# Performance work log

Hardware: AMD Instinct MI355X
Metric: run time of the kernel (lower is better)

The kernel has to match this reference:

```python
import jax, jax.numpy as jnp
import numpy as np

EPS = 1e-5

@jax.custom_vjp
def binarize(x):
    # sign binarization used by Conv2d_1w1a (1-bit weights and activations)
    return jnp.where(x >= 0, 1.0, -1.0).astype(x.dtype)

def _bin_fwd(x):
    return binarize(x), x

def _bin_bwd(x, g):
    # straight-through estimator with hardtanh clipping (standard BNN STE)
    return (g * (jnp.abs(x) <= 1.0).astype(g.dtype),)

binarize.defvjp(_bin_fwd, _bin_bwd)

def setup_inputs() -> dict:
    key = jax.random.key(0)
    k1, k2, k3 = jax.random.split(key, 3)
    B, C_in, H, W = 32, 256, 56, 56
    C_half = 512 // 2
    x = jax.random.normal(k1, (B, C_in, H, W), dtype=jnp.float32)
    gamma = jnp.ones((C_in,), dtype=jnp.float32)
    beta = jnp.zeros((C_in,), dtype=jnp.float32)
    w1 = jax.random.normal(k2, (C_half, C_in), dtype=jnp.float32) * 0.05
    w2 = jax.random.normal(k3, (C_half, C_in), dtype=jnp.float32) * 0.05
    return {"x": x, "gamma": gamma, "beta": beta, "w1": w1, "w2": w2}

def reference(x, gamma, beta, w1, w2):
    # BatchNorm2d (training mode: batch statistics, biased variance)
    mean = jnp.mean(x, axis=(0, 2, 3), keepdims=True)
    var = jnp.var(x, axis=(0, 2, 3), keepdims=True)
    xn = (x - mean) * jax.lax.rsqrt(var + EPS)
    xn = xn * gamma[None, :, None, None] + beta[None, :, None, None]

    # binarize activations once; both convs consume the same binarized map
    a = binarize(xn)
    b1 = binarize(w1)  # [C_half, C_in]
    b2 = binarize(w2)

    # 1x1 stride-2 conv == strided slice + channel contraction
    a1 = a[:, :, ::2, ::2]      # conv_1 path
    a2 = a[:, :, 1::2, 1::2]    # conv_2 path on out[:, :, 1:, 1:]

    out1 = jnp.einsum('bchw,oc->bohw', a1, b1)
    out2 = jnp.einsum('bchw,oc->bohw', a2, b2)
    return jnp.concatenate([out1, out2], axis=1)
```

## Files before the change

kernel.cpp:

```cpp
#include <hip/hip_runtime.h>
#include <stdint.h>

#define CIN 256
#define HW  3136
#define HW4 784
#define NB  32
#define NHO 28
#define NWO 28

__global__ void k_stats_partial(const float* __restrict__ x, double* __restrict__ part) {
    int blk = blockIdx.x;
    int c = blk >> 3;
    int chunk = blk & 7;
    int tid = threadIdx.x;
    double s = 0.0, sq = 0.0;
    for (int bq = 0; bq < 4; ++bq) {
        int b = chunk * 4 + bq;
        const float4* base = (const float4*)x + (size_t)(b * CIN + c) * HW4;
        for (int i = tid; i < HW4; i += 256) {
            float4 v = base[i];
            double a0 = v.x, a1 = v.y, a2 = v.z, a3 = v.w;
            s  += (a0 + a1) + (a2 + a3);
            sq += (a0*a0 + a1*a1) + (a2*a2 + a3*a3);
        }
    }
    __shared__ double ls[256], lq[256];
    ls[tid] = s; lq[tid] = sq;
    __syncthreads();
    for (int off = 128; off > 0; off >>= 1) {
        if (tid < off) { ls[tid] += ls[tid+off]; lq[tid] += lq[tid+off]; }
        __syncthreads();
    }
    if (tid == 0) {
        part[blk*2]   = ls[0];
        part[blk*2+1] = lq[0];
    }
}

__global__ void k_finalize(const double* __restrict__ part,
                           const float* __restrict__ gamma, const float* __restrict__ beta,
                           const float* __restrict__ w1, const float* __restrict__ w2,
                           double* __restrict__ mean_d, double* __restrict__ sg_d,
                           double* __restrict__ beta_d,
                           unsigned long long* __restrict__ wp) {
    int blk = blockIdx.x;
    int tid = threadIdx.x;
    if (blk == 512) {
        int c = tid;
        double s = 0.0, sq = 0.0;
        for (int k = 0; k < 8; ++k) {
            s  += part[(c*8+k)*2];
            sq += part[(c*8+k)*2+1];
        }
        const double n = 100352.0;
        double mean = s / n;
        double var  = sq / n - mean*mean;
        if (var < 0.0) var = 0.0;
        double invstd = 1.0 / sqrt(var + 1e-5);
        mean_d[c] = mean;
        sg_d[c]   = invstd * (double)gamma[c];
        beta_d[c] = (double)beta[c];
    } else {
        int wave = tid >> 6, l = tid & 63;
        int w_idx = blk * 4 + wave;
        int p = w_idx >> 10;
        int rem = w_idx & 1023;
        int o = rem >> 2, wv = rem & 3;
        const float* w = p ? w2 : w1;
        float v = w[o*256 + wv*64 + l];
        unsigned long long m = __ballot(v >= 0.0f);
        if (l == 0) wp[w_idx] = m;
    }
}

__global__ void k_binpack(const float* __restrict__ x,
                          const double* __restrict__ mean_d, const double* __restrict__ sg_d,
                          const double* __restrict__ beta_d,
                          unsigned long long* __restrict__ ap) {
    __shared__ double smean[256], ssg[256], sbeta[256];
    __shared__ unsigned char pred[256*116];
    int blk = blockIdx.x;
    int b = blk / NHO, ho = blk % NHO;
    int tid = threadIdx.x;
    smean[tid] = mean_d[tid]; ssg[tid] = sg_d[tid]; sbeta[tid] = beta_d[tid];
    __syncthreads();

    uint32_t* pred32 = (uint32_t*)pred;
    #pragma unroll 4
    for (int k = 0; k < 28; ++k) {
        int i4 = tid + k*256;
        int c  = i4 / 28;
        int r4 = i4 - c*28;
        float4 v = ((const float4*)x)[(size_t)(b*CIN + c)*HW4 + ho*28 + r4];
        double m = smean[c], sg = ssg[c], bt = sbeta[c];
        uint32_t bits = 0;
        bits |= (((double)v.x - m)*sg + bt >= 0.0) ? 0x00000001u : 0u;
        bits |= (((double)v.y - m)*sg + bt >= 0.0) ? 0x00000100u : 0u;
        bits |= (((double)v.z - m)*sg + bt >= 0.0) ? 0x00010000u : 0u;
        bits |= (((double)v.w - m)*sg + bt >= 0.0) ? 0x01000000u : 0u;
        pred32[c*29 + r4] = bits;
    }
    __syncthreads();

    int g = tid >> 6, l = tid & 63;
    int c = g*64 + l;
    for (int p = 0; p < 2; ++p) {
        for (int wo = 0; wo < NWO; ++wo) {
            unsigned char pr = pred[c*116 + p*57 + 2*wo];
            unsigned long long mask = __ballot(pr != 0);
            if (l == 0)
                ap[(size_t)(((p*NB + b)*NHO + ho)*NWO + wo)*4 + g] = mask;
        }
    }
}

__global__ void k_bingemm(const unsigned long long* __restrict__ ap,
                          const unsigned long long* __restrict__ wp,
                          float* __restrict__ out) {
    __shared__ unsigned long long wl[2048];
    int tid = threadIdx.x;
    for (int k = tid; k < 2048; k += 256) wl[k] = wp[k];
    int blk = blockIdx.x;
    int b = blk / NHO, ho = blk % NHO;
    int o_sub = tid >> 5, wi = tid & 31;
    bool act = wi < NWO;
    unsigned long long a0[2][4];
    if (act) {
        for (int p = 0; p < 2; ++p)
            #pragma unroll
            for (int j = 0; j < 4; ++j)
                a0[p][j] = ap[(size_t)(((p*NB + b)*NHO + ho)*NWO + wi)*4 + j];
    }
    __syncthreads();
    if (!act) return;
    for (int p = 0; p < 2; ++p) {
        size_t outbase = ((size_t)(b*512 + p*256) * 784) + (size_t)ho*NWO + wi;
        #pragma unroll 4
        for (int og = 0; og < 32; ++og) {
            int o = og*8 + o_sub;
            const unsigned long long* w = &wl[p*1024 + o*4];
            int d = __popcll(a0[p][0]^w[0]) + __popcll(a0[p][1]^w[1])
                  + __popcll(a0[p][2]^w[2]) + __popcll(a0[p][3]^w[3]);
            out[outbase + (size_t)o*784] = (float)(256 - 2*d);
        }
    }
}

extern "C" void kernel_launch(void* const* d_in, const int* in_sizes, int n_in,
                              void* d_out, int out_size, void* d_ws, size_t ws_size,
                              hipStream_t stream) {
    const float* x     = (const float*)d_in[0];
    const float* gamma = (const float*)d_in[1];
    const float* beta  = (const float*)d_in[2];
    const float* w1    = (const float*)d_in[3];
    const float* w2    = (const float*)d_in[4];
    float* out = (float*)d_out;

    char* ws = (char*)d_ws;
    double* part   = (double*)ws;
    double* mean_d = (double*)(ws + 32768);
    double* sg_d   = (double*)(ws + 34816);
    double* beta_d = (double*)(ws + 36864);
    unsigned long long* wp = (unsigned long long*)(ws + 40960);
    unsigned long long* ap = (unsigned long long*)(ws + 57344);

    k_stats_partial<<<2048, 256, 0, stream>>>(x, part);
    k_finalize<<<513, 256, 0, stream>>>(part, gamma, beta, w1, w2, mean_d, sg_d, beta_d, wp);
    k_binpack<<<NB*NHO, 256, 0, stream>>>(x, mean_d, sg_d, beta_d, ap);
    k_bingemm<<<NB*NHO, 256, 0, stream>>>(ap, wp, out);
}
```

Baseline: 216.4 us.

## Fuse four kernels into two: stats+weight pack, then finalize+binpack+popcount GEMM

Weight bit-packing moves into the stats kernel as extra blocks. BN finalize, activation bit-packing and the XNOR-popcount GEMM merge into one kernel that keeps packed activations in shared memory instead of a global round trip. Only the strided pixels actually used are kept in the shared predicate buffer, which shrinks its footprint. Each fused block now recomputes the per-channel finalize redundantly and holds more shared memory, which may reduce occupancy.

Measured after the change: 206.0 us. 4.8% less time.

```diff
diff --git a/kernel.cpp b/kernel.cpp
--- a/kernel.cpp
+++ b/kernel.cpp
@@ -2,139 +2,129 @@
 #include <stdint.h>
 
 #define CIN 256
-#define HW  3136
 #define HW4 784
 #define NB  32
 #define NHO 28
 #define NWO 28
 
-__global__ void k_stats_partial(const float* __restrict__ x, double* __restrict__ part) {
+__global__ __launch_bounds__(256) void k_stage1(const float* __restrict__ x,
+                          const float* __restrict__ w1, const float* __restrict__ w2,
+                          double* __restrict__ part, unsigned long long* __restrict__ wp) {
     int blk = blockIdx.x;
-    int c = blk >> 3;
-    int chunk = blk & 7;
     int tid = threadIdx.x;
-    double s = 0.0, sq = 0.0;
-    for (int bq = 0; bq < 4; ++bq) {
-        int b = chunk * 4 + bq;
-        const float4* base = (const float4*)x + (size_t)(b * CIN + c) * HW4;
-        for (int i = tid; i < HW4; i += 256) {
-            float4 v = base[i];
-            double a0 = v.x, a1 = v.y, a2 = v.z, a3 = v.w;
-            s  += (a0 + a1) + (a2 + a3);
-            sq += (a0*a0 + a1*a1) + (a2*a2 + a3*a3);
+    if (blk < 2048) {
+        int c = blk >> 3, chunk = blk & 7;
+        double s = 0.0, sq = 0.0;
+        for (int bq = 0; bq < 4; ++bq) {
+            int b = chunk * 4 + bq;
+            const float4* base = (const float4*)x + (size_t)(b * CIN + c) * HW4;
+            for (int i = tid; i < HW4; i += 256) {
+                float4 v = base[i];
+                double a0 = v.x, a1 = v.y, a2 = v.z, a3 = v.w;
+                s  += (a0 + a1) + (a2 + a3);
+                sq += (a0*a0 + a1*a1) + (a2*a2 + a3*a3);
+            }
         }
-    }
-    __shared__ double ls[256], lq[256];
-    ls[tid] = s; lq[tid] = sq;
-    __syncthreads();
-    for (int off = 128; off > 0; off >>= 1) {
-        if (tid < off) { ls[tid] += ls[tid+off]; lq[tid] += lq[tid+off]; }
+        __shared__ double ls[256], lq[256];
+        ls[tid] = s; lq[tid] = sq;
         __syncthreads();
-    }
-    if (tid == 0) {
-        part[blk*2]   = ls[0];
-        part[blk*2+1] = lq[0];
+        for (int off = 128; off > 0; off >>= 1) {
+            if (tid < off) { ls[tid] += ls[tid+off]; lq[tid] += lq[tid+off]; }
+            __syncthreads();
+        }
+        if (tid == 0) {
+            part[(chunk*256 + c)*2]   = ls[0];
+            part[(chunk*256 + c)*2+1] = lq[0];
+        }
+    } else {
+        int wave = tid >> 6, l = tid & 63;
+        int baseTask = ((blk - 2048)*4 + wave)*4;
+        #pragma unroll
+        for (int t = 0; t < 4; ++t) {
+            int w_idx = baseTask + t;
+            int p = w_idx >> 10, rem = w_idx & 1023;
+            int o = rem >> 2, wv = rem & 3;
+            const float* w = p ? w2 : w1;
+            float v = w[o*256 + wv*64 + l];
+            unsigned long long m = __ballot(v >= 0.0f);
+            if (l == 0) wp[w_idx] = m;
+        }
     }
 }
 
-__global__ void k_finalize(const double* __restrict__ part,
-                           const float* __restrict__ gamma, const float* __restrict__ beta,
-                           const float* __restrict__ w1, const float* __restrict__ w2,
-                           double* __restrict__ mean_d, double* __restrict__ sg_d,
-                           double* __restrict__ beta_d,
-                           unsigned long long* __restrict__ wp) {
+__global__ __launch_bounds__(256) void k_fused(const float* __restrict__ x,
+    const double* __restrict__ part, const float* __restrict__ gamma,
+    const float* __restrict__ beta, const unsigned long long* __restrict__ wp,
+    float* __restrict__ out) {
+    __shared__ double sm[256], ssg[256], sbt[256];
+    __shared__ unsigned char pred[256*60];
+    __shared__ unsigned long long wl[2048];
+    __shared__ unsigned long long apl[224];
     int blk = blockIdx.x;
+    int b = blk / NHO, ho = blk % NHO;
     int tid = threadIdx.x;
-    if (blk == 512) {
+
+    {
+        const ulonglong2* src = (const ulonglong2*)wp;
+        ulonglong2* dst = (ulonglong2*)wl;
+        for (int k = tid; k < 1024; k += 256) dst[k] = src[k];
+    }
+    {
         int c = tid;
         double s = 0.0, sq = 0.0;
         for (int k = 0; k < 8; ++k) {
-            s  += part[(c*8+k)*2];
-            sq += part[(c*8+k)*2+1];
+            s  += part[(k*256 + c)*2];
+            sq += part[(k*256 + c)*2+1];
         }
         const double n = 100352.0;
         double mean = s / n;
         double var  = sq / n - mean*mean;
         if (var < 0.0) var = 0.0;
         double invstd = 1.0 / sqrt(var + 1e-5);
-        mean_d[c] = mean;
-        sg_d[c]   = invstd * (double)gamma[c];
-        beta_d[c] = (double)beta[c];
-    } else {
-        int wave = tid >> 6, l = tid & 63;
-        int w_idx = blk * 4 + wave;
-        int p = w_idx >> 10;
-        int rem = w_idx & 1023;
-        int o = rem >> 2, wv = rem & 3;
-        const float* w = p ? w2 : w1;
-        float v = w[o*256 + wv*64 + l];
-        unsigned long long m = __ballot(v >= 0.0f);
-        if (l == 0) wp[w_idx] = m;
+        sm[c] = mean; ssg[c] = invstd * (double)gamma[c]; sbt[c] = (double)beta[c];
     }
-}
-
-__global__ void k_binpack(const float* __restrict__ x,
-                          const double* __restrict__ mean_d, const double* __restrict__ sg_d,
-                          const double* __restrict__ beta_d,
-                          unsigned long long* __restrict__ ap) {
-    __shared__ double smean[256], ssg[256], sbeta[256];
-    __shared__ unsigned char pred[256*116];
-    int blk = blockIdx.x;
-    int b = blk / NHO, ho = blk % NHO;
-    int tid = threadIdx.x;
-    smean[tid] = mean_d[tid]; ssg[tid] = sg_d[tid]; sbeta[tid] = beta_d[tid];
     __syncthreads();
 
-    uint32_t* pred32 = (uint32_t*)pred;
     #pragma unroll 4
     for (int k = 0; k < 28; ++k) {
         int i4 = tid + k*256;
-        int c  = i4 / 28;
-        int r4 = i4 - c*28;
+        int c = i4 / 28, r4 = i4 - c*28;
         float4 v = ((const float4*)x)[(size_t)(b*CIN + c)*HW4 + ho*28 + r4];
-        double m = smean[c], sg = ssg[c], bt = sbeta[c];
-        uint32_t bits = 0;
-        bits |= (((double)v.x - m)*sg + bt >= 0.0) ? 0x00000001u : 0u;
-        bits |= (((double)v.y - m)*sg + bt >= 0.0) ? 0x00000100u : 0u;
-        bits |= (((double)v.z - m)*sg + bt >= 0.0) ? 0x00010000u : 0u;
-        bits |= (((double)v.w - m)*sg + bt >= 0.0) ? 0x01000000u : 0u;
-        pred32[c*29 + r4] = bits;
+        double m = sm[c], sg = ssg[c], bt = sbt[c];
+        unsigned short bits; int off;
+        if (r4 < 14) {
+            bits  = (((double)v.x - m)*sg + bt >= 0.0) ? 1u : 0u;
+            bits |= (((double)v.z - m)*sg + bt >= 0.0) ? 0x100u : 0u;
+            off = c*60 + 2*r4;
+        } else {
+            bits  = (((double)v.y - m)*sg + bt >= 0.0) ? 1u : 0u;
+            bits |= (((double)v.w - m)*sg + bt >= 0.0) ? 0x100u : 0u;
+            off = c*60 + 28 + 2*(r4 - 14);
+        }
+        *(unsigned short*)&pred[off] = bits;
     }
     __syncthreads();
 
-    int g = tid >> 6, l = tid & 63;
-    int c = g*64 + l;
-    for (int p = 0; p < 2; ++p) {
-        for (int wo = 0; wo < NWO; ++wo) {
-            unsigned char pr = pred[c*116 + p*57 + 2*wo];
-            unsigned long long mask = __ballot(pr != 0);
-            if (l == 0)
-                ap[(size_t)(((p*NB + b)*NHO + ho)*NWO + wo)*4 + g] = mask;
-        }
-    }
-}
-
-__global__ void k_bingemm(const unsigned long long* __restrict__ ap,
-                          const unsigned long long* __restrict__ wp,
-                          float* __restrict__ out) {
-    __shared__ unsigned long long wl[2048];
-    int tid = threadIdx.x;
-    for (int k = tid; k < 2048; k += 256) wl[k] = wp[k];
-    int blk = blockIdx.x;
-    int b = blk / NHO, ho = blk % NHO;
-    int o_sub = tid >> 5, wi = tid & 31;
-    bool act = wi < NWO;
-    unsigned long long a0[2][4];
-    if (act) {
+    {
+        int g = tid >> 6, l = tid & 63;
+        int c = g*64 + l;
         for (int p = 0; p < 2; ++p)
-            #pragma unroll
-            for (int j = 0; j < 4; ++j)
-                a0[p][j] = ap[(size_t)(((p*NB + b)*NHO + ho)*NWO + wi)*4 + j];
+            for (int wo = 0; wo < NWO; ++wo) {
+                unsigned char pr = pred[c*60 + p*28 + wo];
+                unsigned long long mask = __ballot(pr != 0);
+                if (l == 0) apl[p*112 + wo*4 + g] = mask;
+            }
     }
     __syncthreads();
-    if (!act) return;
+
+    int o_sub = tid >> 5, wi = tid & 31;
+    if (wi >= NWO) return;
+    unsigned long long a0[2][4];
+    for (int p = 0; p < 2; ++p)
+        #pragma unroll
+        for (int j = 0; j < 4; ++j) a0[p][j] = apl[p*112 + wi*4 + j];
     for (int p = 0; p < 2; ++p) {
-        size_t outbase = ((size_t)(b*512 + p*256) * 784) + (size_t)ho*NWO + wi;
+        size_t outbase = ((size_t)(b*512 + p*256))*784 + (size_t)ho*NWO + wi;
         #pragma unroll 4
         for (int og = 0; og < 32; ++og) {
             int o = og*8 + o_sub;
@@ -157,15 +147,9 @@
     float* out = (float*)d_out;
 
     char* ws = (char*)d_ws;
-    double* part   = (double*)ws;
-    double* mean_d = (double*)(ws + 32768);
-    double* sg_d   = (double*)(ws + 34816);
-    double* beta_d = (double*)(ws + 36864);
+    double* part = (double*)ws;
     unsigned long long* wp = (unsigned long long*)(ws + 40960);
-    unsigned long long* ap = (unsigned long long*)(ws + 57344);
 
-    k_stats_partial<<<2048, 256, 0, stream>>>(x, part);
-    k_finalize<<<513, 256, 0, stream>>>(part, gamma, beta, w1, w2, mean_d, sg_d, beta_d, wp);
-    k_binpack<<<NB*NHO, 256, 0, stream>>>(x, mean_d, sg_d, beta_d, ap);
-    k_bingemm<<<NB*NHO, 256, 0, stream>>>(ap, wp, out);
+    k_stage1<<<2176, 256, 0, stream>>>(x, w1, w2, part, wp);
+    k_fused<<<NB*NHO, 256, 0, stream>>>(x, part, gamma, beta, wp, out);
 }
```
